# Kernel optimization log

Measured on AMD Instinct MI355X. Metric: run time of the kernel, lower is better.

The kernel has to match this reference:

```python
import jax, jax.numpy as jnp
import numpy as np

B, T, L, H, P = 256, 2048, 4, 64, 1  # batch, seq_len, layers, hidden_size, proj_size(=input_size)


def setup_inputs() -> dict:
    key = jax.random.key(0)
    ks = jax.random.split(key, 6)
    s = 0.1  # keep recurrent dynamics stable
    return {
        "y": jax.random.normal(ks[0], (B, T, P), jnp.float32),
        "W_ih": jax.random.normal(ks[1], (L, 4 * H, P), jnp.float32) * s,
        "W_hh": jax.random.normal(ks[2], (L, 4 * H, P), jnp.float32) * s,
        "b_ih": jax.random.normal(ks[3], (L, 4 * H), jnp.float32) * s,
        "b_hh": jax.random.normal(ks[4], (L, 4 * H), jnp.float32) * s,
        "W_hr": jax.random.normal(ks[5], (L, P, H), jnp.float32) * s,
        "min_seq_len": 1,
    }


def _lstm_layer(x, wih, whh, bih, bhh, whr):
    # x: [B, T, in]; torch gate order: i, f, g, o. proj_size: h = W_hr @ (o * tanh(c)).
    Bq = x.shape[0]
    hid = whh.shape[0] // 4
    gx = jnp.einsum('bti,gi->btg', x, wih) + bih + bhh  # [B, T, 4H], input GEMM batched over time
    h0 = jnp.zeros((Bq, whr.shape[0]), x.dtype)  # projected hidden [B, P]
    c0 = jnp.zeros((Bq, hid), x.dtype)           # cell [B, H]

    def step(carry, g_t):
        h, c = carry
        g = g_t + h @ whh.T  # [B, 4H]
        i, f, gg, o = jnp.split(g, 4, axis=-1)
        c = jax.nn.sigmoid(f) * c + jax.nn.sigmoid(i) * jnp.tanh(gg)
        h = (jax.nn.sigmoid(o) * jnp.tanh(c)) @ whr.T  # project H -> P
        return (h, c), h

    _, hs = jax.lax.scan(step, (h0, c0), jnp.swapaxes(gx, 0, 1))  # time-major scan
    return jnp.swapaxes(hs, 0, 1)  # [B, T, P]


def reference(y, W_ih, W_hh, b_ih, b_hh, W_hr, min_seq_len):
    x = y
    for l in range(W_ih.shape[0]):  # static layer loop (4 layers)
        x = _lstm_layer(x, W_ih[l], W_hh[l], b_ih[l], b_hh[l], W_hr[l])
    return x[:, min_seq_len:]  # matches self.layer(y)[0][:, min_seq_len:]
```

## Files before the change

### kernel.cpp

```cpp
#include <hip/hip_runtime.h>

#define BATCH  256
#define SEQT   2048
#define LAYERS 4
#define HID    64
#define CHUNK  16
#define PHASES (SEQT / CHUNK + LAYERS - 1)

#define LOG2E  1.4426950408889634f
#define K2     (2.0f * LOG2E)

__device__ __forceinline__ float fast_rcp(float x) {
    return __builtin_amdgcn_rcpf(x);
}
__device__ __forceinline__ float fast_exp2(float x) {
    return __builtin_amdgcn_exp2f(x);
}

#define DPP_ADD(v, ctrl)                                                     \
    (v) += __int_as_float(__builtin_amdgcn_update_dpp(                       \
        0, __float_as_int(v), (ctrl), 0xF, 0xF, true))

__device__ __forceinline__ float wave_sum_lane63(float v) {
    DPP_ADD(v, 0x111);
    DPP_ADD(v, 0x112);
    DPP_ADD(v, 0x114);
    DPP_ADD(v, 0x118);
    DPP_ADD(v, 0x142);
    DPP_ADD(v, 0x143);
    return v;
}

__global__ __launch_bounds__(256, 1) void lstm_pipeline_kernel(
    const float* __restrict__ y,
    const float* __restrict__ W_ih,
    const float* __restrict__ W_hh,
    const float* __restrict__ b_ih,
    const float* __restrict__ b_hh,
    const float* __restrict__ W_hr,
    const int*  __restrict__ msl_p,
    float* __restrict__ out)
{
    const int b   = blockIdx.x;
    const int tid = threadIdx.x;
    const int l   = tid >> 6;
    const int k   = tid & 63;
    const int msl = *msl_p;

    __shared__ float y_lds[SEQT];
    __shared__ float out_lds[SEQT];
    __shared__ __align__(16) float h_buf[2][LAYERS][CHUNK];

    {
        const float4* y4  = (const float4*)(y + (size_t)b * SEQT);
        float4*       yl4 = (float4*)y_lds;
        #pragma unroll
        for (int i = tid; i < SEQT / 4; i += 256) yl4[i] = y4[i];
    }

    const int wbase = l * 4 * HID;
    const float wi0 = -LOG2E * W_ih[wbase + 0 * HID + k];
    const float wi1 = -LOG2E * W_ih[wbase + 1 * HID + k];
    const float wi2 =  K2    * W_ih[wbase + 2 * HID + k];
    const float wi3 = -LOG2E * W_ih[wbase + 3 * HID + k];
    const float wh0 = -LOG2E * W_hh[wbase + 0 * HID + k];
    const float wh1 = -LOG2E * W_hh[wbase + 1 * HID + k];
    const float wh2 =  K2    * W_hh[wbase + 2 * HID + k];
    const float wh3 = -LOG2E * W_hh[wbase + 3 * HID + k];
    const float bb0 = -LOG2E * (b_ih[wbase + 0 * HID + k] + b_hh[wbase + 0 * HID + k]);
    const float bb1 = -LOG2E * (b_ih[wbase + 1 * HID + k] + b_hh[wbase + 1 * HID + k]);
    const float bb2 =  K2    * (b_ih[wbase + 2 * HID + k] + b_hh[wbase + 2 * HID + k]);
    const float bb3 = -LOG2E * (b_ih[wbase + 3 * HID + k] + b_hh[wbase + 3 * HID + k]);
    const float wr  = W_hr[l * HID + k];

    float h = 0.0f;
    float C = 0.0f;

    for (int p = 0; p < PHASES; ++p) {
        __syncthreads();
        const int t0 = (p - l) * CHUNK;
        if (t0 >= 0 && t0 < SEQT) {
            float4 xv[CHUNK / 4];
            if (l == 0) {
                const float4* ys = (const float4*)&y_lds[t0];
                #pragma unroll
                for (int q = 0; q < CHUNK / 4; ++q) xv[q] = ys[q];
            } else {
                const float4* hb = (const float4*)&h_buf[(p - 1) & 1][l - 1][0];
                #pragma unroll
                for (int q = 0; q < CHUNK / 4; ++q) xv[q] = hb[q];
            }
            float xs[CHUNK];
            #pragma unroll
            for (int q = 0; q < CHUNK / 4; ++q) {
                xs[4 * q + 0] = xv[q].x; xs[4 * q + 1] = xv[q].y;
                xs[4 * q + 2] = xv[q].z; xs[4 * q + 3] = xv[q].w;
            }

            float p0[CHUNK], p1[CHUNK], p2[CHUNK], p3[CHUNK];
            #pragma unroll
            for (int j = 0; j < CHUNK; ++j) {
                p0[j] = fmaf(xs[j], wi0, bb0);
                p1[j] = fmaf(xs[j], wi1, bb1);
                p2[j] = fmaf(xs[j], wi2, bb2);
                p3[j] = fmaf(xs[j], wi3, bb3);
            }

            float hcol = 0.0f;

            #pragma unroll
            for (int j = 0; j < CHUNK; ++j) {
                const float gi = fmaf(h, wh0, p0[j]);
                const float gf = fmaf(h, wh1, p1[j]);
                const float gg = fmaf(h, wh2, p2[j]);
                const float go = fmaf(h, wh3, p3[j]);

                const float Ei = fast_exp2(gi);
                const float Ef = fast_exp2(gf);
                const float Eg = fast_exp2(gg);
                const float Eo = fast_exp2(go);

                const float ai     = 1.0f + Ei;
                const float ag     = 1.0f + Eg;
                const float af     = 1.0f + Ef;
                const float den_ig = ai * ag;
                const float tg     = fmaf(K2, Eg, -K2);
                const float tgf    = tg * af;
                const float num    = fmaf(C, den_ig, tgf);
                const float den    = den_ig * af;
                C = num * fast_rcp(den);

                const float Ec   = fast_exp2(C);
                const float ao   = 1.0f + Eo;
                const float ac   = 1.0f + Ec;
                const float den2 = ao * ac;
                const float num2 = fmaf(wr, Ec, -wr);
                const float v    = num2 * fast_rcp(den2);

                const float vs = wave_sum_lane63(v);

                h = __int_as_float(
                    __builtin_amdgcn_readlane(__float_as_int(vs), 63));

                hcol = (k == j) ? h : hcol;
            }

            if (k < CHUNK) {
                if (l < LAYERS - 1) h_buf[p & 1][l][k] = hcol;
                else                out_lds[t0 + k]    = hcol;
            }
        }
    }

    __syncthreads();
    const int nout = SEQT - msl;
    float* outb = out + (size_t)b * nout;
    for (int i = tid; i < nout; i += 256) outb[i] = out_lds[i + msl];
}

extern "C" void kernel_launch(void* const* d_in, const int* in_sizes, int n_in,
                              void* d_out, int out_size, void* d_ws, size_t ws_size,
                              hipStream_t stream) {
    const float* y    = (const float*)d_in[0];
    const float* W_ih = (const float*)d_in[1];
    const float* W_hh = (const float*)d_in[2];
    const float* b_ih = (const float*)d_in[3];
    const float* b_hh = (const float*)d_in[4];
    const float* W_hr = (const float*)d_in[5];
    const int*   msl  = (const int*)d_in[6];
    float* out = (float*)d_out;

    lstm_pipeline_kernel<<<BATCH, 256, 0, stream>>>(
        y, W_ih, W_hh, b_ih, b_hh, W_hr, msl, out);
}
```

Measured before the change: 319.7 us.

## Process two batch elements per block to raise waves per CU

Each block now handles two batch sequences, with 8 waves (4 layers × 2 batches), and the grid is halved. The aim is to interleave two independent latency-bound recurrence chains on each SIMD to hide exp/rcp/DPP latency. In exchange, only half as many blocks are launched, so on a 256-CU device half the CUs may sit idle. The block-wide barrier also now synchronizes twice as many waves.

Result: slower. 455.6 us (+42.5%).

```diff
diff --git a/kernel.cpp b/kernel.cpp
--- a/kernel.cpp
+++ b/kernel.cpp
@@ -6,6 +6,9 @@
 #define HID    64
 #define CHUNK  16
 #define PHASES (SEQT / CHUNK + LAYERS - 1)
+#define BPB    2
+#define GRID   (BATCH / BPB)
+#define NTHR   (BPB * LAYERS * 64)
 
 #define LOG2E  1.4426950408889634f
 #define K2     (2.0f * LOG2E)
@@ -31,7 +34,7 @@
     return v;
 }
 
-__global__ __launch_bounds__(256, 1) void lstm_pipeline_kernel(
+__global__ __launch_bounds__(NTHR, 1) void lstm_pipeline_kernel(
     const float* __restrict__ y,
     const float* __restrict__ W_ih,
     const float* __restrict__ W_hh,
@@ -41,21 +44,25 @@
     const int*  __restrict__ msl_p,
     float* __restrict__ out)
 {
-    const int b   = blockIdx.x;
     const int tid = threadIdx.x;
-    const int l   = tid >> 6;
+    const int w   = tid >> 6;
+    const int bi  = w >> 2;
+    const int l   = w & 3;
     const int k   = tid & 63;
+    const int b   = blockIdx.x * BPB + bi;
     const int msl = *msl_p;
 
-    __shared__ float y_lds[SEQT];
-    __shared__ float out_lds[SEQT];
-    __shared__ __align__(16) float h_buf[2][LAYERS][CHUNK];
+    __shared__ float y_lds[BPB][SEQT];
+    __shared__ float out_lds[BPB][SEQT];
+    __shared__ __align__(16) float h_buf[2][BPB][LAYERS][CHUNK];
 
     {
-        const float4* y4  = (const float4*)(y + (size_t)b * SEQT);
-        float4*       yl4 = (float4*)y_lds;
+        const int sb = tid >> 8;
+        const int st = tid & 255;
+        const float4* y4  = (const float4*)(y + (size_t)(blockIdx.x * BPB + sb) * SEQT);
+        float4*       yl4 = (float4*)&y_lds[sb][0];
         #pragma unroll
-        for (int i = tid; i < SEQT / 4; i += 256) yl4[i] = y4[i];
+        for (int i = st; i < SEQT / 4; i += 256) yl4[i] = y4[i];
     }
 
     const int wbase = l * 4 * HID;
@@ -82,11 +89,11 @@
         if (t0 >= 0 && t0 < SEQT) {
             float4 xv[CHUNK / 4];
             if (l == 0) {
-                const float4* ys = (const float4*)&y_lds[t0];
+                const float4* ys = (const float4*)&y_lds[bi][t0];
                 #pragma unroll
                 for (int q = 0; q < CHUNK / 4; ++q) xv[q] = ys[q];
             } else {
-                const float4* hb = (const float4*)&h_buf[(p - 1) & 1][l - 1][0];
+                const float4* hb = (const float4*)&h_buf[(p - 1) & 1][bi][l - 1][0];
                 #pragma unroll
                 for (int q = 0; q < CHUNK / 4; ++q) xv[q] = hb[q];
             }
@@ -146,16 +153,18 @@
             }
 
             if (k < CHUNK) {
-                if (l < LAYERS - 1) h_buf[p & 1][l][k] = hcol;
-                else                out_lds[t0 + k]    = hcol;
+                if (l < LAYERS - 1) h_buf[p & 1][bi][l][k] = hcol;
+                else                out_lds[bi][t0 + k]    = hcol;
             }
         }
     }
 
     __syncthreads();
     const int nout = SEQT - msl;
-    float* outb = out + (size_t)b * nout;
-    for (int i = tid; i < nout; i += 256) outb[i] = out_lds[i + msl];
+    const int fb   = tid >> 8;
+    const int ft   = tid & 255;
+    float* outb = out + (size_t)(blockIdx.x * BPB + fb) * nout;
+    for (int i = ft; i < nout; i += 256) outb[i] = out_lds[fb][i + msl];
 }
 
 extern "C" void kernel_launch(void* const* d_in, const int* in_sizes, int n_in,
@@ -170,6 +179,6 @@
     const int*   msl  = (const int*)d_in[6];
     float* out = (float*)d_out;
 
-    lstm_pipeline_kernel<<<BATCH, 256, 0, stream>>>(
+    lstm_pipeline_kernel<<<GRID, NTHR, 0, stream>>>(
         y, W_ih, W_hh, b_ih, b_hh, W_hr, msl, out);
 }
```
